# Optimization experiments

Measured on AMD Instinct MI355X. Metric: run time of the kernel, lower is better.

## Reference

```python
import jax, jax.numpy as jnp
import numpy as np
from jax import lax

B, N, S, K, C = 8, 4096, 1024, 64, 64
RADIUS = 0.2
MLP = [64, 128, 256]
INT_MAX = jnp.iinfo(jnp.int32).max

_batched_gather = jax.vmap(lambda a, i: a[i])  # (N,D),(S,K)->(S,K,D)


def setup_inputs() -> dict:
    key = jax.random.key(0)
    ks = jax.random.split(key, 6)
    xyz = jax.random.uniform(ks[0], (B, N, 3), dtype=jnp.float32)
    points = jax.random.normal(ks[1], (B, N, C), dtype=jnp.float32)
    fps_inds = jax.random.randint(ks[2], (B, S), 0, N, dtype=jnp.int32)
    c_in = [3 + C] + MLP[:-1]
    w0 = jax.random.normal(ks[3], (c_in[0], MLP[0]), dtype=jnp.float32) * 0.1
    w1 = jax.random.normal(ks[4], (c_in[1], MLP[1]), dtype=jnp.float32) * 0.1
    w2 = jax.random.normal(ks[5], (c_in[2], MLP[2]), dtype=jnp.float32) * 0.1
    return {"xyz": xyz, "points": points, "fps_inds": fps_inds,
            "w0": w0, "w1": w1, "w2": w2}


def _query_ball_point(radius, nsample, xyz, new_xyz):
    # dists: (B, S, N)
    dists = jnp.linalg.norm(new_xyz[:, :, None, :] - xyz[:, None, :, :], axis=-1)
    # nsample nearest neighbors (ascending distance), like argsort[:, :, :nsample]
    neg_d, idx = lax.top_k(-dists, nsample)            # (B,S,K)
    valid = (-neg_d) < radius                          # prefix mask (dists ascending)
    idx_m = jnp.where(valid, idx, INT_MAX)
    sidx = jnp.sort(idx_m, axis=-1)
    # invalid slots -> first (smallest) valid index
    return jnp.where(valid, sidx, sidx[:, :, :1])


def reference(xyz, points, fps_inds, w0, w1, w2):
    new_xyz = _batched_gather(xyz, fps_inds)                       # (B,S,3)
    idx = _query_ball_point(RADIUS, K, xyz, new_xyz)               # (B,S,K)
    grouped_xyz = _batched_gather(xyz, idx) - new_xyz[:, :, None]  # (B,S,K,3)
    grouped_pts = _batched_gather(points, idx)                     # (B,S,K,C)
    feat = jnp.concatenate([grouped_xyz, grouped_pts], axis=-1)    # (B,S,K,3+C)
    for w in (w0, w1, w2):  # 1x1 conv == channel matmul, then relu
        feat = jax.nn.relu(jnp.einsum('bskc,cf->bskf', feat, w))
    new_points = jnp.max(feat, axis=2)                             # (B,S,F)
    return new_xyz, new_points
```

## Files before the change

kernel.cpp:

```cpp
#include <hip/hip_runtime.h>

#define NB 8
#define NN 4096
#define NS 1024
#define NC 64
#define OUT_PTS_OFF (NB*NS*3)
#define CAP2 256
#define RB 0.2f
#define QPB 4

typedef __attribute__((ext_vector_type(8))) short bf16x8;
typedef __attribute__((ext_vector_type(4))) float f32x4;
typedef unsigned long long u64;

static __device__ __forceinline__ short f2bf(float f){
  unsigned u = __float_as_uint(f);
  unsigned r = (u + 0x7FFFu + ((u>>16)&1u)) >> 16;
  return (short)r;
}
static __device__ __forceinline__ float bf2f(short s){
  return __uint_as_float(((unsigned)(unsigned short)s) << 16);
}
static __device__ __forceinline__ unsigned cvtpk(float a, float b){
  unsigned r;
  asm("v_cvt_pk_bf16_f32 %0, %1, %2" : "=v"(r) : "v"(a), "v"(b));
  return r;
}

#define WS_PX1_SH   1048576
#define WS_WF_SH    3145728

__global__ __launch_bounds__(256) void prep_grid(
    const float* __restrict__ w0, const float* __restrict__ w1,
    const float* __restrict__ w2, short* __restrict__ ws,
    const float* __restrict__ xyz, float4* __restrict__ gxyz,
    int* __restrict__ cstart)
{
  __shared__ int hist[125];
  __shared__ int base[125];
  const int tid = threadIdx.x;

  if (blockIdx.x < 184) {
    int e = blockIdx.x*256 + tid;
    if (e >= 47104) return;
    float v = 0.f;
    if (e < 6144) {
      int j=e&7, l=(e>>3)&63, nt=(e>>9)&3, kt=e>>11;
      int k = kt*32 + ((l>>4)<<3) + j, n = nt*16 + (l&15);
      if (k < 64) v = w0[(3+k)*64 + n];
      else if (k < 67) v = w0[(k-64)*64 + n];
    } else if (e < 14336) {
      int e2=e-6144;
      int j=e2&7, l=(e2>>3)&63, nt=(e2>>9)&7, kt=e2>>12;
      int k = kt*32 + ((l>>4)<<3) + j, n = nt*16 + (l&15);
      v = w1[k*128 + n];
    } else {
      int e3=e-14336;
      int j=e3&7, l=(e3>>3)&63, nt=(e3>>9)&15, kt=e3>>13;
      int k = (kt*2 + (j&1))*16 + ((l>>4)<<2) + (j>>1);
      v = w2[k*256 + nt*16 + (l&15)];
    }
    ws[e] = f2bf(v);
    return;
  }

  const int b = blockIdx.x - 184;
  const float* xb = xyz + (size_t)b*NN*3;
  if (tid < 125) hist[tid] = 0;
  __syncthreads();

  float xs[16], ys[16], zs[16]; int cl[16];
  {
    const float4* xv = (const float4*)(xb + tid*48);
    #pragma unroll
    for (int g=0; g<4; ++g) {
      float4 v0 = xv[g*3], v1 = xv[g*3+1], v2 = xv[g*3+2];
      xs[g*4+0]=v0.x; xs[g*4+1]=v0.w; xs[g*4+2]=v1.z; xs[g*4+3]=v2.y;
      ys[g*4+0]=v0.y; ys[g*4+1]=v1.x; ys[g*4+2]=v1.w; ys[g*4+3]=v2.z;
      zs[g*4+0]=v0.z; zs[g*4+1]=v1.y; zs[g*4+2]=v2.x; zs[g*4+3]=v2.w;
    }
  }
  #pragma unroll
  for (int r=0; r<16; ++r) {
    int cx = min(4, (int)(xs[r]*5.0f));
    int cy = min(4, (int)(ys[r]*5.0f));
    int cz = min(4, (int)(zs[r]*5.0f));
    cl[r] = (cz*5+cy)*5+cx;
    atomicAdd(&hist[cl[r]], 1);
  }
  __syncthreads();
  if (tid == 0) {
    int acc = 0;
    for (int c=0; c<125; ++c) { base[c]=acc; cstart[b*128+c]=acc; acc+=hist[c]; }
    cstart[b*128+125] = NN;
  }
  __syncthreads();
  #pragma unroll
  for (int r=0; r<16; ++r) {
    int slot = atomicAdd(&base[cl[r]], 1);
    gxyz[b*NN + slot] = make_float4(xs[r], ys[r], zs[r], __int_as_float(tid*16+r));
  }
}

__global__ __launch_bounds__(256) void px1_select(
    const float* __restrict__ xyz, const float* __restrict__ points,
    const int* __restrict__ fps_inds, const short* __restrict__ wsb,
    const float4* __restrict__ gxyz, const int* __restrict__ cstart,
    short* __restrict__ px1, unsigned short* __restrict__ gsidx,
    float* __restrict__ out)
{
  __shared__ u64 candk[4][CAP2];
  __shared__ int tmpi[4][64];
  __shared__ int segS[4][28], segB[4][28], segE[4][28];
  __shared__ int scell[126];

  const int tid = threadIdx.x;

  if (blockIdx.x < 512) {
    const int w = tid>>6, l = tid&63, lr = l&15, grp = l>>4;
    const int rowbase = blockIdx.x*64 + w*16;
    const int row = rowbase + lr;
    const float* prow = points + (size_t)row*NC;
    const float* xr   = xyz + (size_t)row*3;

    bf16x8 a0, a1, a2;
    {
      float4 u0 = *(const float4*)(prow + grp*8);
      float4 u1 = *(const float4*)(prow + grp*8 + 4);
      float4 u2 = *(const float4*)(prow + 32 + grp*8);
      float4 u3 = *(const float4*)(prow + 32 + grp*8 + 4);
      a0 = (bf16x8){f2bf(u0.x),f2bf(u0.y),f2bf(u0.z),f2bf(u0.w),f2bf(u1.x),f2bf(u1.y),f2bf(u1.z),f2bf(u1.w)};
      a1 = (bf16x8){f2bf(u2.x),f2bf(u2.y),f2bf(u2.z),f2bf(u2.w),f2bf(u3.x),f2bf(u3.y),f2bf(u3.z),f2bf(u3.w)};
      short e0=0,e1=0,e2v=0;
      if (grp==0) { e0=f2bf(xr[0]); e1=f2bf(xr[1]); e2v=f2bf(xr[2]); }
      a2 = (bf16x8){e0,e1,e2v,0,0,0,0,0};
    }
    f32x4 zero4 = {0.f,0.f,0.f,0.f};
    #pragma unroll
    for (int nt=0; nt<4; ++nt) {
      f32x4 acc = zero4;
      bf16x8 b0 = *(const bf16x8*)(wsb + (((0*4+nt)*64 + l)<<3));
      bf16x8 b1 = *(const bf16x8*)(wsb + (((1*4+nt)*64 + l)<<3));
      bf16x8 b2 = *(const bf16x8*)(wsb + (((2*4+nt)*64 + l)<<3));
      acc = __builtin_amdgcn_mfma_f32_16x16x32_bf16(a0, b0, acc, 0,0,0);
      acc = __builtin_amdgcn_mfma_f32_16x16x32_bf16(a1, b1, acc, 0,0,0);
      acc = __builtin_amdgcn_mfma_f32_16x16x32_bf16(a2, b2, acc, 0,0,0);
      #pragma unroll
      for (int i=0;i<4;++i)
        px1[(size_t)(rowbase + grp*4 + i)*64 + nt*16 + lr] = f2bf(acc[i]);
    }
    return;
  }

  const int sb = blockIdx.x - 512;
  const int wv = tid>>6, lane = tid&63;
  const int q = sb*QPB + wv, b = q >> 10;
  const float* xb = xyz + (size_t)b*NN*3;

  if (tid < 126) scell[tid] = cstart[b*128+tid];
  __syncthreads();

  const int fps = fps_inds[q];
  const float qx = xb[fps*3+0], qy = xb[fps*3+1], qz = xb[fps*3+2];
  if (lane < 3) out[q*3+lane] = xb[fps*3+lane];

  int len = 0, s = 0;
  if (lane < 27) {
    const int cx = min(4, (int)(qx*5.0f));
    const int cy = min(4, (int)(qy*5.0f));
    const int cz = min(4, (int)(qz*5.0f));
    int ncx = cx + lane%3 - 1, ncy = cy + (lane/3)%3 - 1, ncz = cz + lane/9 - 1;
    if (ncx>=0 && ncx<5 && ncy>=0 && ncy<5 && ncz>=0 && ncz<5) {
      float lox = ncx*0.2f - 1e-5f, hix = lox + 0.2f + 2e-5f;
      float loy = ncy*0.2f - 1e-5f, hiy = loy + 0.2f + 2e-5f;
      float loz = ncz*0.2f - 1e-5f, hiz = loz + 0.2f + 2e-5f;
      float dx = fmaxf(0.f, fmaxf(lox-qx, qx-hix));
      float dy = fmaxf(0.f, fmaxf(loy-qy, qy-hiy));
      float dz = fmaxf(0.f, fmaxf(loz-qz, qz-hiz));
      if (fmaf(dx,dx, fmaf(dy,dy, dz*dz)) <= 0.0402f) {
        int c = (ncz*5+ncy)*5+ncx;
        s = scell[c]; len = scell[c+1] - s;
      }
    }
  }
  int incl = len;
  #pragma unroll
  for (int off=1; off<64; off<<=1) {
    int v = __shfl_up(incl, off, 64);
    if (lane >= off) incl += v;
  }
  const int T = __shfl(incl, 26, 64);
  if (lane < 27) { segS[wv][lane]=s; segB[wv][lane]=incl-len; segE[wv][lane]=incl; }
  __builtin_amdgcn_wave_barrier();

  const float4* gb = gxyz + b*NN;
  int base = 0, k = 0;
  const int rounds = (T + 63) >> 6;
  const u64 ltmask = (1ull << lane) - 1ull;
  for (int r = 0; r < rounds; ++r) {
    int t = r*64 + lane;
    bool hit = false; u64 key = 0;
    if (t < T) {
      while (t >= segE[wv][k]) ++k;
      float4 p = gb[segS[wv][k] + (t - segB[wv][k])];
      float fx = qx-p.x, fy = qy-p.y, fz = qz-p.z;
      float ff = fmaf(fx,fx, fmaf(fy,fy, fz*fz));
      if (ff < 0.0402f) {
        float dx=__fsub_rn(qx,p.x), dy=__fsub_rn(qy,p.y), dz=__fsub_rn(qz,p.z);
        float d2=__fadd_rn(__fadd_rn(__fmul_rn(dx,dx),__fmul_rn(dy,dy)),__fmul_rn(dz,dz));
        float d = __fsqrt_rn(d2);
        if (d < RB) {
          hit = true;
          key = ((u64)__float_as_uint(d) << 16) | (u64)(unsigned)__float_as_int(p.w);
        }
      }
    }
    u64 m = __ballot(hit);
    int pos = base + (int)__popcll(m & ltmask);
    if (hit && pos < CAP2) candk[wv][pos] = key;
    base += (int)__popcll(m);
  }
  int cnt = base < CAP2 ? base : CAP2;
  __builtin_amdgcn_wave_barrier();

  if (cnt > 64) {
    for (int j = lane; j < cnt; j += 64) {
      u64 kj = candk[wv][j];
      int rk = 0;
      for (int i = 0; i < cnt; ++i) rk += (int)(candk[wv][i] < kj);
      if (rk < 64) tmpi[wv][rk] = (int)(kj & 0xFFFFu);
    }
    __builtin_amdgcn_wave_barrier();
    int v = tmpi[wv][lane];
    int p = 0;
    #pragma unroll 8
    for (int u = 0; u < 64; ++u) p += (int)(tmpi[wv][u] < v);
    gsidx[q*64 + p] = (unsigned short)v;
  } else {
    if (lane < cnt) {
      int v = (int)(candk[wv][lane] & 0xFFFFu);
      int p = 0;
      for (int u = 0; u < cnt; ++u) p += (int)((int)(candk[wv][u] & 0xFFFFu) < v);
      tmpi[wv][p] = v;
    }
    __builtin_amdgcn_wave_barrier();
    gsidx[q*64 + lane] = (unsigned short)tmpi[wv][lane < cnt ? lane : 0];
  }
}

__global__ __launch_bounds__(256,2) void mlp_kernel(
    const float* __restrict__ xyz, const int* __restrict__ fps_inds,
    const float* __restrict__ w0, const short* __restrict__ wsb,
    const short* __restrict__ px1, const unsigned short* __restrict__ gsidx,
    float* __restrict__ out)
{
  __shared__ __align__(16) short w1s[8192];
  __shared__ __align__(16) short h2f[8192];
  __shared__ float q1s[QPB][64];
  __shared__ int sidx[QPB][64];

  const int tid = threadIdx.x;
  const int w = tid>>6, l = tid&63, lr = l&15, grp = l>>4;
  const int q0 = blockIdx.x*QPB;
  const int b = q0 >> 10;
  const float* xb = xyz + (size_t)b*NN*3;

  bf16x8 b3[4][4];
  #pragma unroll
  for (int kt=0; kt<4; ++kt)
    #pragma unroll
    for (int j=0; j<4; ++j)
      b3[kt][j] = *(const bf16x8*)(wsb + 14336 + (((kt*16 + w*4 + j)*64 + l)<<3));

  #pragma unroll
  for (int e = 0; e < 4; ++e) {
    int s = tid + e*256;
    *(bf16x8*)&w1s[s*8] = *(const bf16x8*)(wsb + 6144 + s*8);
  }
  {
    int qq = tid>>6, t = tid&63;
    int fp = fps_inds[q0+qq];
    sidx[qq][t] = (int)gsidx[(q0+qq)*64 + t];
    q1s[qq][t] = xb[fp*3]*w0[t] + xb[fp*3+1]*w0[64+t] + xb[fp*3+2]*w0[128+t];
  }
  if (tid < QPB*3) {
    int qq = tid/3, c = tid - qq*3;
    int fp = fps_inds[q0+qq];
    out[(q0+qq)*3 + c] = xb[fp*3+c];
  }
  __syncthreads();

  const short* px1b = px1 + (size_t)b*NN*64;
  const int myrow = w*16 + lr;

  bf16x8 v0, v1;
  {
    int idx = sidx[0][myrow];
    v0 = *(const bf16x8*)(px1b + idx*64 + grp*8);
    v1 = *(const bf16x8*)(px1b + idx*64 + 32 + grp*8);
  }

  f32x4 zero4 = {0.f,0.f,0.f,0.f};
  const int uu4 = (lr>>2) << 4;
  const int gg4 = grp << 4;

  for (int qq = 0; qq < QPB; ++qq) {
    if (qq) __syncthreads();

    bf16x8 a20, a21;
    {
      union { unsigned u[4]; bf16x8 v; } ua, ub;
      #pragma unroll
      for (int jp=0; jp<4; ++jp) {
        float x0 = fmaxf(bf2f(v0[2*jp  ]) - q1s[qq][grp*8+2*jp  ], 0.f);
        float x1 = fmaxf(bf2f(v0[2*jp+1]) - q1s[qq][grp*8+2*jp+1], 0.f);
        ua.u[jp] = cvtpk(x0, x1);
        float y0 = fmaxf(bf2f(v1[2*jp  ]) - q1s[qq][32+grp*8+2*jp  ], 0.f);
        float y1 = fmaxf(bf2f(v1[2*jp+1]) - q1s[qq][32+grp*8+2*jp+1], 0.f);
        ub.u[jp] = cvtpk(y0, y1);
      }
      a20 = ua.v; a21 = ub.v;
    }
    if (qq+1 < QPB) {
      int idx = sidx[qq+1][myrow];
      v0 = *(const bf16x8*)(px1b + idx*64 + grp*8);
      v1 = *(const bf16x8*)(px1b + idx*64 + 32 + grp*8);
    }

    #pragma unroll
    for (int ntp=0; ntp<4; ++ntp) {
      f32x4 accA = zero4, accB = zero4;
      bf16x8 bA0 = *(const bf16x8*)&w1s[((0*8 + 2*ntp  )*64 + l)*8];
      bf16x8 bA1 = *(const bf16x8*)&w1s[((1*8 + 2*ntp  )*64 + l)*8];
      bf16x8 bB0 = *(const bf16x8*)&w1s[((0*8 + 2*ntp+1)*64 + l)*8];
      bf16x8 bB1 = *(const bf16x8*)&w1s[((1*8 + 2*ntp+1)*64 + l)*8];
      accA = __builtin_amdgcn_mfma_f32_16x16x32_bf16(a20, bA0, accA, 0,0,0);
      accA = __builtin_amdgcn_mfma_f32_16x16x32_bf16(a21, bA1, accA, 0,0,0);
      accB = __builtin_amdgcn_mfma_f32_16x16x32_bf16(a20, bB0, accB, 0,0,0);
      accB = __builtin_amdgcn_mfma_f32_16x16x32_bf16(a21, bB1, accB, 0,0,0);
      #pragma unroll
      for (int i=0; i<4; ++i) {
        unsigned pv = cvtpk(fmaxf(accA[i],0.f), fmaxf(accB[i],0.f));
        int byteoff = ((((w*4+ntp)*64 + (lr>>2)*16 + grp*4 + i)<<4) + ((lr&3)<<2)) ^ uu4;
        *(unsigned*)((char*)h2f + byteoff) = pv;
      }
    }
    __syncthreads();

    float rm[4][4];
    #pragma unroll
    for (int j=0;j<4;++j)
      #pragma unroll
      for (int i=0;i<4;++i) rm[j][i] = 0.f;
    #pragma unroll
    for (int mt=0; mt<4; ++mt) {
      f32x4 acc[4] = {zero4, zero4, zero4, zero4};
      #pragma unroll
      for (int kt=0; kt<4; ++kt) {
        int byteoff = ((((mt*4+kt)*64 + l)<<4)) ^ gg4;
        bf16x8 a = *(const bf16x8*)((const char*)h2f + byteoff);
        #pragma unroll
        for (int j=0; j<4; ++j)
          acc[j] = __builtin_amdgcn_mfma_f32_16x16x32_bf16(a, b3[kt][j], acc[j], 0,0,0);
      }
      #pragma unroll
      for (int j=0; j<4; ++j)
        #pragma unroll
        for (int i=0; i<4; ++i) rm[j][i] = fmaxf(rm[j][i], acc[j][i]);
    }
    #pragma unroll
    for (int j=0; j<4; ++j) {
      float m = fmaxf(fmaxf(rm[j][0],rm[j][1]), fmaxf(rm[j][2],rm[j][3]));
      m = fmaxf(m, __shfl_xor(m, 16, 64));
      m = fmaxf(m, __shfl_xor(m, 32, 64));
      if (grp == 0) out[OUT_PTS_OFF + (q0+qq)*256 + (w*4+j)*16 + lr] = m;
    }
  }
}

extern "C" void kernel_launch(void* const* d_in, const int* in_sizes, int n_in,
                              void* d_out, int out_size, void* d_ws, size_t ws_size,
                              hipStream_t stream) {
  const float* xyz      = (const float*)d_in[0];
  const float* points   = (const float*)d_in[1];
  const int*   fps_inds = (const int*)d_in[2];
  const float* w0       = (const float*)d_in[3];
  const float* w1       = (const float*)d_in[4];
  const float* w2       = (const float*)d_in[5];
  float* out = (float*)d_out;

  unsigned short* gsidx = (unsigned short*)d_ws;
  float4* gxyz  = (float4*)((char*)d_ws + 1048576);
  int*    cstart= (int*)((char*)d_ws + 1572864);
  short*  px1   = (short*)d_ws + WS_PX1_SH;
  short*  wsb   = (short*)d_ws + WS_WF_SH;

  hipLaunchKernelGGL(prep_grid,  dim3(192), dim3(256), 0, stream,
                     w0, w1, w2, wsb, xyz, gxyz, cstart);
  hipLaunchKernelGGL(px1_select, dim3(512 + NB*NS/QPB), dim3(256), 0, stream,
                     xyz, points, fps_inds, wsb, gxyz, cstart, px1, gsidx, out);
  hipLaunchKernelGGL(mlp_kernel, dim3(NB*NS/QPB), dim3(256), 0, stream,
                     xyz, fps_inds, w0, wsb, px1, gsidx, out);
}
```

Before: 92.24 us.

## Fuse ball-query neighbor selection into MLP kernel, keep indices in shared memory

```diff
diff --git a/kernel.cpp b/kernel.cpp
--- a/kernel.cpp
+++ b/kernel.cpp
@@ -102,165 +102,66 @@
   }
 }
 
-__global__ __launch_bounds__(256) void px1_select(
+__global__ __launch_bounds__(256) void px1_kernel(
     const float* __restrict__ xyz, const float* __restrict__ points,
-    const int* __restrict__ fps_inds, const short* __restrict__ wsb,
-    const float4* __restrict__ gxyz, const int* __restrict__ cstart,
-    short* __restrict__ px1, unsigned short* __restrict__ gsidx,
-    float* __restrict__ out)
+    const short* __restrict__ wsb, short* __restrict__ px1)
 {
-  __shared__ u64 candk[4][CAP2];
-  __shared__ int tmpi[4][64];
-  __shared__ int segS[4][28], segB[4][28], segE[4][28];
-  __shared__ int scell[126];
-
   const int tid = threadIdx.x;
-
-  if (blockIdx.x < 512) {
-    const int w = tid>>6, l = tid&63, lr = l&15, grp = l>>4;
-    const int rowbase = blockIdx.x*64 + w*16;
-    const int row = rowbase + lr;
-    const float* prow = points + (size_t)row*NC;
-    const float* xr   = xyz + (size_t)row*3;
-
-    bf16x8 a0, a1, a2;
-    {
-      float4 u0 = *(const float4*)(prow + grp*8);
-      float4 u1 = *(const float4*)(prow + grp*8 + 4);
-      float4 u2 = *(const float4*)(prow + 32 + grp*8);
-      float4 u3 = *(const float4*)(prow + 32 + grp*8 + 4);
-      a0 = (bf16x8){f2bf(u0.x),f2bf(u0.y),f2bf(u0.z),f2bf(u0.w),f2bf(u1.x),f2bf(u1.y),f2bf(u1.z),f2bf(u1.w)};
-      a1 = (bf16x8){f2bf(u2.x),f2bf(u2.y),f2bf(u2.z),f2bf(u2.w),f2bf(u3.x),f2bf(u3.y),f2bf(u3.z),f2bf(u3.w)};
-      short e0=0,e1=0,e2v=0;
-      if (grp==0) { e0=f2bf(xr[0]); e1=f2bf(xr[1]); e2v=f2bf(xr[2]); }
-      a2 = (bf16x8){e0,e1,e2v,0,0,0,0,0};
-    }
-    f32x4 zero4 = {0.f,0.f,0.f,0.f};
-    #pragma unroll
-    for (int nt=0; nt<4; ++nt) {
-      f32x4 acc = zero4;
-      bf16x8 b0 = *(const bf16x8*)(wsb + (((0*4+nt)*64 + l)<<3));
-      bf16x8 b1 = *(const bf16x8*)(wsb + (((1*4+nt)*64 + l)<<3));
-      bf16x8 b2 = *(const bf16x8*)(wsb + (((2*4+nt)*64 + l)<<3));
-      acc = __builtin_amdgcn_mfma_f32_16x16x32_bf16(a0, b0, acc, 0,0,0);
-      acc = __builtin_amdgcn_mfma_f32_16x16x32_bf16(a1, b1, acc, 0,0,0);
-      acc = __builtin_amdgcn_mfma_f32_16x16x32_bf16(a2, b2, acc, 0,0,0);
-      #pragma unroll
-      for (int i=0;i<4;++i)
-        px1[(size_t)(rowbase + grp*4 + i)*64 + nt*16 + lr] = f2bf(acc[i]);
-    }
-    return;
-  }
-
-  const int sb = blockIdx.x - 512;
-  const int wv = tid>>6, lane = tid&63;
-  const int q = sb*QPB + wv, b = q >> 10;
-  const float* xb = xyz + (size_t)b*NN*3;
-
-  if (tid < 126) scell[tid] = cstart[b*128+tid];
-  __syncthreads();
-
-  const int fps = fps_inds[q];
-  const float qx = xb[fps*3+0], qy = xb[fps*3+1], qz = xb[fps*3+2];
-  if (lane < 3) out[q*3+lane] = xb[fps*3+lane];
-
-  int len = 0, s = 0;
-  if (lane < 27) {
-    const int cx = min(4, (int)(qx*5.0f));
-    const int cy = min(4, (int)(qy*5.0f));
-    const int cz = min(4, (int)(qz*5.0f));
-    int ncx = cx + lane%3 - 1, ncy = cy + (lane/3)%3 - 1, ncz = cz + lane/9 - 1;
-    if (ncx>=0 && ncx<5 && ncy>=0 && ncy<5 && ncz>=0 && ncz<5) {
-      float lox = ncx*0.2f - 1e-5f, hix = lox + 0.2f + 2e-5f;
-      float loy = ncy*0.2f - 1e-5f, hiy = loy + 0.2f + 2e-5f;
-      float loz = ncz*0.2f - 1e-5f, hiz = loz + 0.2f + 2e-5f;
-      float dx = fmaxf(0.f, fmaxf(lox-qx, qx-hix));
-      float dy = fmaxf(0.f, fmaxf(loy-qy, qy-hiy));
-      float dz = fmaxf(0.f, fmaxf(loz-qz, qz-hiz));
-      if (fmaf(dx,dx, fmaf(dy,dy, dz*dz)) <= 0.0402f) {
-        int c = (ncz*5+ncy)*5+ncx;
-        s = scell[c]; len = scell[c+1] - s;
-      }
-    }
-  }
-  int incl = len;
-  #pragma unroll
-  for (int off=1; off<64; off<<=1) {
-    int v = __shfl_up(incl, off, 64);
-    if (lane >= off) incl += v;
-  }
-  const int T = __shfl(incl, 26, 64);
-  if (lane < 27) { segS[wv][lane]=s; segB[wv][lane]=incl-len; segE[wv][lane]=incl; }
-  __builtin_amdgcn_wave_barrier();
-
-  const float4* gb = gxyz + b*NN;
-  int base = 0, k = 0;
-  const int rounds = (T + 63) >> 6;
-  const u64 ltmask = (1ull << lane) - 1ull;
-  for (int r = 0; r < rounds; ++r) {
-    int t = r*64 + lane;
-    bool hit = false; u64 key = 0;
-    if (t < T) {
-      while (t >= segE[wv][k]) ++k;
-      float4 p = gb[segS[wv][k] + (t - segB[wv][k])];
-      float fx = qx-p.x, fy = qy-p.y, fz = qz-p.z;
-      float ff = fmaf(fx,fx, fmaf(fy,fy, fz*fz));
-      if (ff < 0.0402f) {
-        float dx=__fsub_rn(qx,p.x), dy=__fsub_rn(qy,p.y), dz=__fsub_rn(qz,p.z);
-        float d2=__fadd_rn(__fadd_rn(__fmul_rn(dx,dx),__fmul_rn(dy,dy)),__fmul_rn(dz,dz));
-        float d = __fsqrt_rn(d2);
-        if (d < RB) {
-          hit = true;
-          key = ((u64)__float_as_uint(d) << 16) | (u64)(unsigned)__float_as_int(p.w);
-        }
-      }
-    }
-    u64 m = __ballot(hit);
-    int pos = base + (int)__popcll(m & ltmask);
-    if (hit && pos < CAP2) candk[wv][pos] = key;
-    base += (int)__popcll(m);
-  }
-  int cnt = base < CAP2 ? base : CAP2;
-  __builtin_amdgcn_wave_barrier();
-
-  if (cnt > 64) {
-    for (int j = lane; j < cnt; j += 64) {
-      u64 kj = candk[wv][j];
-      int rk = 0;
-      for (int i = 0; i < cnt; ++i) rk += (int)(candk[wv][i] < kj);
-      if (rk < 64) tmpi[wv][rk] = (int)(kj & 0xFFFFu);
-    }
-    __builtin_amdgcn_wave_barrier();
-    int v = tmpi[wv][lane];
-    int p = 0;
-    #pragma unroll 8
-    for (int u = 0; u < 64; ++u) p += (int)(tmpi[wv][u] < v);
-    gsidx[q*64 + p] = (unsigned short)v;
-  } else {
-    if (lane < cnt) {
-      int v = (int)(candk[wv][lane] & 0xFFFFu);
-      int p = 0;
-      for (int u = 0; u < cnt; ++u) p += (int)((int)(candk[wv][u] & 0xFFFFu) < v);
-      tmpi[wv][p] = v;
-    }
-    __builtin_amdgcn_wave_barrier();
-    gsidx[q*64 + lane] = (unsigned short)tmpi[wv][lane < cnt ? lane : 0];
-  }
-}
-
-__global__ __launch_bounds__(256,2) void mlp_kernel(
+  const int w = tid>>6, l = tid&63, lr = l&15, grp = l>>4;
+  const int rowbase = blockIdx.x*64 + w*16;
+  const int row = rowbase + lr;
+  const float* prow = points + (size_t)row*NC;
+  const float* xr   = xyz + (size_t)row*3;
+
+  bf16x8 a0, a1, a2;
+  {
+    float4 u0 = *(const float4*)(prow + grp*8);
+    float4 u1 = *(const float4*)(prow + grp*8 + 4);
+    float4 u2 = *(const float4*)(prow + 32 + grp*8);
+    float4 u3 = *(const float4*)(prow + 32 + grp*8 + 4);
+    a0 = (bf16x8){f2bf(u0.x),f2bf(u0.y),f2bf(u0.z),f2bf(u0.w),f2bf(u1.x),f2bf(u1.y),f2bf(u1.z),f2bf(u1.w)};
+    a1 = (bf16x8){f2bf(u2.x),f2bf(u2.y),f2bf(u2.z),f2bf(u2.w),f2bf(u3.x),f2bf(u3.y),f2bf(u3.z),f2bf(u3.w)};
+    short e0=0,e1=0,e2v=0;
+    if (grp==0) { e0=f2bf(xr[0]); e1=f2bf(xr[1]); e2v=f2bf(xr[2]); }
+    a2 = (bf16x8){e0,e1,e2v,0,0,0,0,0};
+  }
+  f32x4 zero4 = {0.f,0.f,0.f,0.f};
+  #pragma unroll
+  for (int nt=0; nt<4; ++nt) {
+    f32x4 acc = zero4;
+    bf16x8 b0 = *(const bf16x8*)(wsb + (((0*4+nt)*64 + l)<<3));
+    bf16x8 b1 = *(const bf16x8*)(wsb + (((1*4+nt)*64 + l)<<3));
+    bf16x8 b2 = *(const bf16x8*)(wsb + (((2*4+nt)*64 + l)<<3));
+    acc = __builtin_amdgcn_mfma_f32_16x16x32_bf16(a0, b0, acc, 0,0,0);
+    acc = __builtin_amdgcn_mfma_f32_16x16x32_bf16(a1, b1, acc, 0,0,0);
+    acc = __builtin_amdgcn_mfma_f32_16x16x32_bf16(a2, b2, acc, 0,0,0);
+    #pragma unroll
+    for (int i=0;i<4;++i)
+      px1[(size_t)(rowbase + grp*4 + i)*64 + nt*16 + lr] = f2bf(acc[i]);
+  }
+}
+
+__global__ __launch_bounds__(256,2) void select_mlp(
     const float* __restrict__ xyz, const int* __restrict__ fps_inds,
     const float* __restrict__ w0, const short* __restrict__ wsb,
-    const short* __restrict__ px1, const unsigned short* __restrict__ gsidx,
-    float* __restrict__ out)
+    const short* __restrict__ px1, const float4* __restrict__ gxyz,
+    const int* __restrict__ cstart, float* __restrict__ out)
 {
   __shared__ __align__(16) short w1s[8192];
   __shared__ __align__(16) short h2f[8192];
   __shared__ float q1s[QPB][64];
   __shared__ int sidx[QPB][64];
 
+  u64* candk = (u64*)h2f;
+  int* tmpi  = (int*)((char*)h2f + 8192);
+  int* segS  = (int*)((char*)h2f + 9216);
+  int* segB  = (int*)((char*)h2f + 9664);
+  int* segE  = (int*)((char*)h2f + 10112);
+  int* scell = (int*)((char*)h2f + 10560);
+
   const int tid = threadIdx.x;
-  const int w = tid>>6, l = tid&63, lr = l&15, grp = l>>4;
+  const int wv = tid>>6, l = tid&63, lr = l&15, grp = l>>4;
+  const int lane = l;
   const int q0 = blockIdx.x*QPB;
   const int b = q0 >> 10;
   const float* xb = xyz + (size_t)b*NN*3;
@@ -270,27 +171,110 @@
   for (int kt=0; kt<4; ++kt)
     #pragma unroll
     for (int j=0; j<4; ++j)
-      b3[kt][j] = *(const bf16x8*)(wsb + 14336 + (((kt*16 + w*4 + j)*64 + l)<<3));
+      b3[kt][j] = *(const bf16x8*)(wsb + 14336 + (((kt*16 + wv*4 + j)*64 + l)<<3));
 
   #pragma unroll
   for (int e = 0; e < 4; ++e) {
     int s = tid + e*256;
     *(bf16x8*)&w1s[s*8] = *(const bf16x8*)(wsb + 6144 + s*8);
   }
+  if (tid < 126) scell[tid] = cstart[b*128+tid];
+  __syncthreads();
+
   {
-    int qq = tid>>6, t = tid&63;
-    int fp = fps_inds[q0+qq];
-    sidx[qq][t] = (int)gsidx[(q0+qq)*64 + t];
-    q1s[qq][t] = xb[fp*3]*w0[t] + xb[fp*3+1]*w0[64+t] + xb[fp*3+2]*w0[128+t];
-  }
-  if (tid < QPB*3) {
-    int qq = tid/3, c = tid - qq*3;
-    int fp = fps_inds[q0+qq];
-    out[(q0+qq)*3 + c] = xb[fp*3+c];
+    const int q = q0 + wv;
+    const int fps = fps_inds[q];
+    const float qx = xb[fps*3+0], qy = xb[fps*3+1], qz = xb[fps*3+2];
+    if (lane < 3) out[q*3+lane] = xb[fps*3+lane];
+
+    int len = 0, s = 0;
+    if (lane < 27) {
+      const int cx = min(4, (int)(qx*5.0f));
+      const int cy = min(4, (int)(qy*5.0f));
+      const int cz = min(4, (int)(qz*5.0f));
+      int ncx = cx + lane%3 - 1, ncy = cy + (lane/3)%3 - 1, ncz = cz + lane/9 - 1;
+      if (ncx>=0 && ncx<5 && ncy>=0 && ncy<5 && ncz>=0 && ncz<5) {
+        float lox = ncx*0.2f - 1e-5f, hix = lox + 0.2f + 2e-5f;
+        float loy = ncy*0.2f - 1e-5f, hiy = loy + 0.2f + 2e-5f;
+        float loz = ncz*0.2f - 1e-5f, hiz = loz + 0.2f + 2e-5f;
+        float dx = fmaxf(0.f, fmaxf(lox-qx, qx-hix));
+        float dy = fmaxf(0.f, fmaxf(loy-qy, qy-hiy));
+        float dz = fmaxf(0.f, fmaxf(loz-qz, qz-hiz));
+        if (fmaf(dx,dx, fmaf(dy,dy, dz*dz)) <= 0.0402f) {
+          int c = (ncz*5+ncy)*5+ncx;
+          s = scell[c]; len = scell[c+1] - s;
+        }
+      }
+    }
+    int incl = len;
+    #pragma unroll
+    for (int off=1; off<64; off<<=1) {
+      int v = __shfl_up(incl, off, 64);
+      if (lane >= off) incl += v;
+    }
+    const int T = __shfl(incl, 26, 64);
+    if (lane < 27) { segS[wv*28+lane]=s; segB[wv*28+lane]=incl-len; segE[wv*28+lane]=incl; }
+    __builtin_amdgcn_wave_barrier();
+
+    const float4* gb = gxyz + b*NN;
+    int base = 0, k = 0;
+    const int rounds = (T + 63) >> 6;
+    const u64 ltmask = (1ull << lane) - 1ull;
+    for (int r = 0; r < rounds; ++r) {
+      int t = r*64 + lane;
+      bool hit = false; u64 key = 0;
+      if (t < T) {
+        while (t >= segE[wv*28+k]) ++k;
+        float4 p = gb[segS[wv*28+k] + (t - segB[wv*28+k])];
+        float fx = qx-p.x, fy = qy-p.y, fz = qz-p.z;
+        float ff = fmaf(fx,fx, fmaf(fy,fy, fz*fz));
+        if (ff < 0.0402f) {
+          float dx=__fsub_rn(qx,p.x), dy=__fsub_rn(qy,p.y), dz=__fsub_rn(qz,p.z);
+          float d2=__fadd_rn(__fadd_rn(__fmul_rn(dx,dx),__fmul_rn(dy,dy)),__fmul_rn(dz,dz));
+          float d = __fsqrt_rn(d2);
+          if (d < RB) {
+            hit = true;
+            key = ((u64)__float_as_uint(d) << 16) | (u64)(unsigned)__float_as_int(p.w);
+          }
+        }
+      }
+      u64 m = __ballot(hit);
+      int pos = base + (int)__popcll(m & ltmask);
+      if (hit && pos < CAP2) candk[wv*CAP2 + pos] = key;
+      base += (int)__popcll(m);
+    }
+    int cnt = base < CAP2 ? base : CAP2;
+    __builtin_amdgcn_wave_barrier();
+
+    if (cnt > 64) {
+      for (int j = lane; j < cnt; j += 64) {
+        u64 kj = candk[wv*CAP2 + j];
+        int rk = 0;
+        for (int i = 0; i < cnt; ++i) rk += (int)(candk[wv*CAP2 + i] < kj);
+        if (rk < 64) tmpi[wv*64 + rk] = (int)(kj & 0xFFFFu);
+      }
+      __builtin_amdgcn_wave_barrier();
+      int v = tmpi[wv*64 + lane];
+      int p = 0;
+      #pragma unroll 8
+      for (int u = 0; u < 64; ++u) p += (int)(tmpi[wv*64 + u] < v);
+      sidx[wv][p] = v;
+    } else {
+      if (lane < cnt) {
+        int v = (int)(candk[wv*CAP2 + lane] & 0xFFFFu);
+        int p = 0;
+        for (int u = 0; u < cnt; ++u) p += (int)((int)(candk[wv*CAP2 + u] & 0xFFFFu) < v);
+        tmpi[wv*64 + p] = v;
+      }
+      __builtin_amdgcn_wave_barrier();
+      sidx[wv][lane] = tmpi[wv*64 + (lane < cnt ? lane : 0)];
+    }
+    q1s[wv][lane] = qx*w0[lane] + qy*w0[64+lane] + qz*w0[128+lane];
   }
   __syncthreads();
 
   const short* px1b = px1 + (size_t)b*NN*64;
+  const int w = wv;
   const int myrow = w*16 + lr;
 
   bf16x8 v0, v1;
@@ -389,7 +373,6 @@
   const float* w2       = (const float*)d_in[5];
   float* out = (float*)d_out;
 
-  unsigned short* gsidx = (unsigned short*)d_ws;
   float4* gxyz  = (float4*)((char*)d_ws + 1048576);
   int*    cstart= (int*)((char*)d_ws + 1572864);
   short*  px1   = (short*)d_ws + WS_PX1_SH;
@@ -397,8 +380,8 @@
 
   hipLaunchKernelGGL(prep_grid,  dim3(192), dim3(256), 0, stream,
                      w0, w1, w2, wsb, xyz, gxyz, cstart);
-  hipLaunchKernelGGL(px1_select, dim3(512 + NB*NS/QPB), dim3(256), 0, stream,
-                     xyz, points, fps_inds, wsb, gxyz, cstart, px1, gsidx, out);
-  hipLaunchKernelGGL(mlp_kernel, dim3(NB*NS/QPB), dim3(256), 0, stream,
-                     xyz, fps_inds, w0, wsb, px1, gsidx, out);
-}
+  hipLaunchKernelGGL(px1_kernel, dim3(512), dim3(256), 0, stream,
+                     xyz, points, wsb, px1);
+  hipLaunchKernelGGL(select_mlp, dim3(NB*NS/QPB), dim3(256), 0, stream,
+                     xyz, fps_inds, w0, wsb, px1, gxyz, cstart, out);
+}
```

After: 121.4 us. +31.6%, slower.
